# Kernel optimization log

Hardware: AMD Instinct MI355X
Metric: run time of the kernel (lower is better)

Reference implementation:

```python
import jax, jax.numpy as jnp
import numpy as np

B, S, D = 8, 2048, 512
KD = 64          # key_dim == value_dim
WIDTH = 128      # attention_width
NEG = 1.0e9


def setup_inputs() -> dict:
    key = jax.random.key(0)
    ks = jax.random.split(key, 16)
    glorot_dd = float(np.sqrt(6.0 / (D + KD)))
    glorot_sd = float(np.sqrt(6.0 / (S + KD)))
    u = lambda k, shape, lim: jax.random.uniform(k, shape, jnp.float32, -lim, lim)
    return {
        "x": jax.random.normal(ks[0], (B, S, D), jnp.float32),
        "Wqr": u(ks[1], (D, KD), glorot_dd), "bqr": jnp.zeros((KD,), jnp.float32),
        "Wqi": u(ks[2], (D, KD), glorot_dd), "bqi": jnp.zeros((KD,), jnp.float32),
        "Wkr": u(ks[3], (D, KD), glorot_dd), "bkr": jnp.zeros((KD,), jnp.float32),
        "Wki": u(ks[4], (D, KD), glorot_dd), "bki": jnp.zeros((KD,), jnp.float32),
        "Wv": u(ks[5], (D, KD), glorot_dd),  "bv": jnp.zeros((KD,), jnp.float32),
        "pos_qr": u(ks[6], (S, KD), glorot_sd), "pos_qi": u(ks[7], (S, KD), glorot_sd),
        "pos_kr": u(ks[8], (S, KD), glorot_sd), "pos_ki": u(ks[9], (S, KD), glorot_sd),
        "temperature": jnp.ones((1,), jnp.float32),
    }


def _masks():
    ind = jnp.arange(S)
    band = (jnp.abs(ind[:, None] - ind[None, :]) <= WIDTH).astype(jnp.float32)  # [S,S]
    causal = jnp.tril(jnp.ones((S, S), jnp.float32))                            # [S,S]
    return band, causal


def reference(x, Wqr, bqr, Wqi, bqi, Wkr, bkr, Wki, bki, Wv, bv,
              pos_qr, pos_qi, pos_kr, pos_ki, temperature):
    scale = 1.0 / jnp.sqrt(jnp.float32(KD))
    # complex Q/K via two real Dense layers; Q scaled BEFORE adding interference
    qr = (x @ Wqr + bqr) * scale + pos_qr[None]   # [B,S,KD]
    qi = (x @ Wqi + bqi) * scale + pos_qi[None]
    kr = (x @ Wkr + bkr) + pos_kr[None]
    ki = (x @ Wki + bki) + pos_ki[None]
    v = x @ Wv + bv                                # [B,S,KD]
    # real part of complex Q @ K^T (transpose, not conjugate-transpose)
    scores = (jnp.einsum('bsd,btd->bst', qr, kr)
              - jnp.einsum('bsd,btd->bst', qi, ki)) * scale  # [B,S,S]
    band, causal = _masks()
    scores = scores * band - NEG * (1.0 - band)
    scores = scores * causal - NEG * (1.0 - causal)
    probs = jax.nn.softmax(scores * temperature[0], axis=-1)
    return jnp.einsum('bst,btd->bsd', probs, v)
```

## Files before the change

kernel.cpp:

```cpp
#include <hip/hip_runtime.h>

#define NB 8
#define NS 2048
#define ND 512
#define NKD 64
#define NM (NB*NS)

typedef _Float16 f16x8 __attribute__((ext_vector_type(8)));
typedef float f32x4 __attribute__((ext_vector_type(4)));


__global__ __launch_bounds__(256) void wprep_kernel(
    const float* __restrict__ w0, const float* __restrict__ w1,
    const float* __restrict__ w2, const float* __restrict__ w3,
    const float* __restrict__ w4,
    f16x8* __restrict__ wfrag)
{
    const int t = blockIdx.x * 256 + threadIdx.x;
    const int p    = t >> 12;
    const int nf   = (t >> 10) & 3;
    const int kt   = (t >> 6) & 15;
    const int lane = t & 63;
    const float* __restrict__ W = (p==0)?w0:(p==1)?w1:(p==2)?w2:(p==3)?w3:w4;
    const int n  = nf*16 + (lane & 15);
    const int k0 = kt*32 + (lane >> 4)*8;
    f16x8 v;
    #pragma unroll
    for (int j = 0; j < 8; ++j)
        v[j] = (_Float16)W[(size_t)(k0 + j)*NKD + n];
    wfrag[t] = v;
}

__global__ __launch_bounds__(256) void proj_mfma(
    const float* __restrict__ x,
    const f16x8* __restrict__ wfrag,
    const float* __restrict__ b0, const float* __restrict__ b1,
    const float* __restrict__ b2, const float* __restrict__ b3,
    const float* __restrict__ b4,
    const float* __restrict__ p0, const float* __restrict__ p1,
    const float* __restrict__ p2, const float* __restrict__ p3,
    _Float16* __restrict__ qkri,
    _Float16* __restrict__ vT)
{
    const int g    = (blockIdx.x * 256 + threadIdx.x) >> 6;
    const int lane = threadIdx.x & 63;
    const int m0   = g * 16;

    const int row = m0 + (lane & 15);
    const int kb  = (lane >> 4) * 8;
    const float* __restrict__ xrow = x + (size_t)row * ND + kb;
    const f16x8* __restrict__ wf   = wfrag + lane;

    f32x4 acc[5][4];
    #pragma unroll
    for (int p = 0; p < 5; ++p)
        #pragma unroll
        for (int nf = 0; nf < 4; ++nf) acc[p][nf] = (f32x4){0.f,0.f,0.f,0.f};

    for (int kt = 0; kt < 16; ++kt) {
        float4 xa = *(const float4*)(xrow + kt*32);
        float4 xb = *(const float4*)(xrow + kt*32 + 4);
        f16x8 a;
        a[0]=(_Float16)xa.x; a[1]=(_Float16)xa.y;
        a[2]=(_Float16)xa.z; a[3]=(_Float16)xa.w;
        a[4]=(_Float16)xb.x; a[5]=(_Float16)xb.y;
        a[6]=(_Float16)xb.z; a[7]=(_Float16)xb.w;
        #pragma unroll
        for (int p = 0; p < 5; ++p)
            #pragma unroll
            for (int nf = 0; nf < 4; ++nf) {
                f16x8 b = wf[(p*4 + nf)*1024 + kt*64];
                acc[p][nf] = __builtin_amdgcn_mfma_f32_16x16x32_f16(a, b, acc[p][nf], 0, 0, 0);
            }
    }

    const float* biases[5] = {b0, b1, b2, b3, b4};
    const float* poss[4]   = {p0, p1, p2, p3};

    const int col   = lane & 15;
    const int rbase = (lane >> 4) << 2;
    const int bidx  = m0 >> 11;

    #pragma unroll
    for (int p = 0; p < 4; ++p) {
        _Float16* ob = qkri + ((size_t)p*NM + m0) * NKD;
        #pragma unroll
        for (int nf = 0; nf < 4; ++nf) {
            const int c = nf*16 + col;
            const float bb = biases[p][c];
            #pragma unroll
            for (int r = 0; r < 4; ++r) {
                const int mm = rbase + r;
                const int s  = (m0 + mm) & (NS - 1);
                float t = acc[p][nf][r] + bb;
                if (p < 2) t = t * 0.125f + poss[p][s*NKD + c];
                else       t = t + poss[p][s*NKD + c];
                ob[(size_t)mm*NKD + c] = (_Float16)t;
            }
        }
    }
    {
        _Float16* vb = vT + (size_t)bidx*NKD*NS;
        #pragma unroll
        for (int nf = 0; nf < 4; ++nf) {
            const int c = nf*16 + col;
            const float bb = b4[c];
            #pragma unroll
            for (int r = 0; r < 4; ++r) {
                const int s = (m0 + rbase + r) & (NS - 1);
                vb[(size_t)c*NS + s] = (_Float16)(acc[4][nf][r] + bb);
            }
        }
    }
}

#define PSTR 200

__global__ __launch_bounds__(64) void attn_mfma(
    const _Float16* __restrict__ qkri,
    const _Float16* __restrict__ vT,
    const float* __restrict__ temp,
    float* __restrict__ out)
{
    __shared__ _Float16 pl[16 * PSTR];

    const int lane = threadIdx.x;
    const int i0   = blockIdx.x * 16;
    const int b    = blockIdx.y;
    const int jb   = i0 - 128;

    const _Float16* __restrict__ qr_g = qkri + ((size_t)0*NM + (size_t)b*NS)*NKD;
    const _Float16* __restrict__ qi_g = qkri + ((size_t)1*NM + (size_t)b*NS)*NKD;
    const _Float16* __restrict__ kr_g = qkri + ((size_t)2*NM + (size_t)b*NS)*NKD;
    const _Float16* __restrict__ ki_g = qkri + ((size_t)3*NM + (size_t)b*NS)*NKD;
    const _Float16* __restrict__ vT_b = vT + (size_t)b*NKD*NS;

    const int qrow = i0 + (lane & 15);
    const int d0   = (lane >> 4) * 8;
    f16x8 aqr[2], aqi[2];
    #pragma unroll
    for (int kt = 0; kt < 2; ++kt) {
        aqr[kt] = *(const f16x8*)&qr_g[(size_t)qrow*NKD + kt*32 + d0];
        f16x8 qi8 = *(const f16x8*)&qi_g[(size_t)qrow*NKD + kt*32 + d0];
        aqi[kt] = -qi8;
    }

    const f16x8 zf = {};
    f32x4 st[9];
    #pragma unroll
    for (int t = 0; t < 9; ++t) {
        const int row = jb + 16*t + (lane & 15);
        const bool ok = (row >= 0);
        const _Float16* krp = kr_g + (size_t)row*NKD + d0;
        const _Float16* kip = ki_g + (size_t)row*NKD + d0;
        f16x8 bkr0 = ok ? *(const f16x8*)(krp)      : zf;
        f16x8 bkr1 = ok ? *(const f16x8*)(krp + 32) : zf;
        f16x8 bki0 = ok ? *(const f16x8*)(kip)      : zf;
        f16x8 bki1 = ok ? *(const f16x8*)(kip + 32) : zf;
        f32x4 acc = (f32x4){0.f,0.f,0.f,0.f};
        acc = __builtin_amdgcn_mfma_f32_16x16x32_f16(aqr[0], bkr0, acc, 0,0,0);
        acc = __builtin_amdgcn_mfma_f32_16x16x32_f16(aqr[1], bkr1, acc, 0,0,0);
        acc = __builtin_amdgcn_mfma_f32_16x16x32_f16(aqi[0], bki0, acc, 0,0,0);
        acc = __builtin_amdgcn_mfma_f32_16x16x32_f16(aqi[1], bki1, acc, 0,0,0);
        st[t] = acc;
    }

    const float sT  = 0.125f * temp[0];
    const int col   = lane & 15;
    const int qg4   = (lane >> 4) * 4;
    const int jrmin = -jb;
    float mx[4] = {-3e38f, -3e38f, -3e38f, -3e38f};
    #pragma unroll
    for (int t = 0; t < 9; ++t) {
        const int jr = 16*t + col;
        #pragma unroll
        for (int r = 0; r < 4; ++r) {
            const int row16 = qg4 + r;
            const bool ok = (jr >= row16) && (jr <= 128 + row16) && (jr >= jrmin);
            const float s = ok ? st[t][r]*sT : -1e30f;
            st[t][r] = s;
            mx[r] = fmaxf(mx[r], s);
        }
    }
    #pragma unroll
    for (int off = 1; off < 16; off <<= 1)
        #pragma unroll
        for (int r = 0; r < 4; ++r)
            mx[r] = fmaxf(mx[r], __shfl_xor(mx[r], off, 16));

    float sum[4] = {0.f, 0.f, 0.f, 0.f};
    #pragma unroll
    for (int t = 0; t < 9; ++t)
        #pragma unroll
        for (int r = 0; r < 4; ++r) {
            const float e = __expf(st[t][r] - mx[r]);
            st[t][r] = e;
            sum[r] += e;
        }
    #pragma unroll
    for (int off = 1; off < 16; off <<= 1)
        #pragma unroll
        for (int r = 0; r < 4; ++r)
            sum[r] += __shfl_xor(sum[r], off, 16);
    float inv[4];
    #pragma unroll
    for (int r = 0; r < 4; ++r) inv[r] = 1.0f / sum[r];

    #pragma unroll
    for (int t = 0; t < 9; ++t) {
        const int jr = 16*t + col;
        #pragma unroll
        for (int r = 0; r < 4; ++r)
            pl[(qg4 + r)*PSTR + jr] = (_Float16)(st[t][r] * inv[r]);
    }
    #pragma unroll
    for (int r = 0; r < 4; ++r)
        pl[(qg4 + r)*PSTR + 144 + col] = (_Float16)0.f;
    __syncthreads();

    f32x4 oacc[4];
    #pragma unroll
    for (int nf = 0; nf < 4; ++nf) oacc[nf] = (f32x4){0.f,0.f,0.f,0.f};
    const _Float16* pa = pl + (lane & 15)*PSTR + (lane >> 4)*8;
    #pragma unroll
    for (int kt = 0; kt < 5; ++kt) {
        f16x8 a = *(const f16x8*)(pa + kt*32);
        const int k0 = jb + kt*32 + (lane >> 4)*8;
        const bool okv = (k0 >= 0);
        #pragma unroll
        for (int nf = 0; nf < 4; ++nf) {
            const int d = nf*16 + (lane & 15);
            f16x8 bv = okv ? *(const f16x8*)&vT_b[(size_t)d*NS + k0] : zf;
            oacc[nf] = __builtin_amdgcn_mfma_f32_16x16x32_f16(a, bv, oacc[nf], 0,0,0);
        }
    }

    float* ob = out + ((size_t)b*NS + i0)*NKD;
    #pragma unroll
    for (int nf = 0; nf < 4; ++nf)
        #pragma unroll
        for (int r = 0; r < 4; ++r)
            ob[(size_t)(qg4 + r)*NKD + nf*16 + col] = oacc[nf][r];
}

extern "C" void kernel_launch(void* const* d_in, const int* in_sizes, int n_in,
                              void* d_out, int out_size, void* d_ws, size_t ws_size,
                              hipStream_t stream)
{
    const float* x    = (const float*)d_in[0];
    const float* w0   = (const float*)d_in[1];
    const float* b0   = (const float*)d_in[2];
    const float* w1   = (const float*)d_in[3];
    const float* b1   = (const float*)d_in[4];
    const float* w2   = (const float*)d_in[5];
    const float* b2   = (const float*)d_in[6];
    const float* w3   = (const float*)d_in[7];
    const float* b3   = (const float*)d_in[8];
    const float* w4   = (const float*)d_in[9];
    const float* b4   = (const float*)d_in[10];
    const float* p0   = (const float*)d_in[11];
    const float* p1   = (const float*)d_in[12];
    const float* p2   = (const float*)d_in[13];
    const float* p3   = (const float*)d_in[14];
    const float* temp = (const float*)d_in[15];

    char* ws = (char*)d_ws;
    f16x8*    wfrag = (f16x8*)ws;
    _Float16* qkri  = (_Float16*)(ws + 327680);
    _Float16* vT    = (_Float16*)(ws + 327680 + 8388608);

    wprep_kernel<<<80, 256, 0, stream>>>(w0, w1, w2, w3, w4, wfrag);

    proj_mfma<<<256, 256, 0, stream>>>(x, wfrag,
                                       b0, b1, b2, b3, b4,
                                       p0, p1, p2, p3, qkri, vT);

    dim3 gB(NS/16, NB);
    attn_mfma<<<gB, 64, 0, stream>>>(qkri, vT, temp, (float*)d_out);
}
```

Measured before the change: 46.71 us.

## Split attention block across four waves with LDS score exchange and reduction

Each attention block now runs four wavefronts instead of one. The 9 score tiles and the 5 PV k-steps are divided among the waves. Scores go to shared memory as fp32, every wave recomputes the row max and sum from LDS, and partial PV outputs are summed through LDS by wave 0. The aim is more parallelism and shorter per-wave serial MFMA chains, at the cost of extra LDS traffic, two barriers and redundant softmax-statistics work.

```diff
diff --git a/kernel.cpp b/kernel.cpp
--- a/kernel.cpp
+++ b/kernel.cpp
@@ -114,17 +114,21 @@
     }
 }
 
-#define PSTR 200
-
-__global__ __launch_bounds__(64) void attn_mfma(
+#define SST 164
+#define OST 68
+
+__global__ __launch_bounds__(256) void attn_mfma(
     const _Float16* __restrict__ qkri,
     const _Float16* __restrict__ vT,
     const float* __restrict__ temp,
     float* __restrict__ out)
 {
-    __shared__ _Float16 pl[16 * PSTR];
-
-    const int lane = threadIdx.x;
+    __shared__ __align__(16) float scf[16*SST];
+    __shared__ __align__(16) float olds[3][16*OST];
+
+    const int tid  = threadIdx.x;
+    const int w    = tid >> 6;
+    const int lane = tid & 63;
     const int i0   = blockIdx.x * 16;
     const int b    = blockIdx.y;
     const int jb   = i0 - 128;
@@ -135,8 +139,13 @@
     const _Float16* __restrict__ ki_g = qkri + ((size_t)3*NM + (size_t)b*NS)*NKD;
     const _Float16* __restrict__ vT_b = vT + (size_t)b*NKD*NS;
 
-    const int qrow = i0 + (lane & 15);
-    const int d0   = (lane >> 4) * 8;
+    const f16x8 zf = {};
+    const int col  = lane & 15;
+    const int seg  = lane >> 4;
+    const int qg4  = seg * 4;
+
+    const int qrow = i0 + col;
+    const int d0   = seg * 8;
     f16x8 aqr[2], aqi[2];
     #pragma unroll
     for (int kt = 0; kt < 2; ++kt) {
@@ -145,11 +154,13 @@
         aqi[kt] = -qi8;
     }
 
-    const f16x8 zf = {};
-    f32x4 st[9];
-    #pragma unroll
-    for (int t = 0; t < 9; ++t) {
-        const int row = jb + 16*t + (lane & 15);
+    const float sT  = 0.125f * temp[0];
+    const int jrmin = -jb;
+    const int tA = (w == 0) ? 0 : (2*w + 1);
+    const int tB = 2*w + 2;
+
+    for (int t = tA; t <= tB; ++t) {
+        const int row = jb + 16*t + col;
         const bool ok = (row >= 0);
         const _Float16* krp = kr_g + (size_t)row*NKD + d0;
         const _Float16* kip = ki_g + (size_t)row*NKD + d0;
@@ -162,85 +173,90 @@
         acc = __builtin_amdgcn_mfma_f32_16x16x32_f16(aqr[1], bkr1, acc, 0,0,0);
         acc = __builtin_amdgcn_mfma_f32_16x16x32_f16(aqi[0], bki0, acc, 0,0,0);
         acc = __builtin_amdgcn_mfma_f32_16x16x32_f16(aqi[1], bki1, acc, 0,0,0);
-        st[t] = acc;
-    }
-
-    const float sT  = 0.125f * temp[0];
-    const int col   = lane & 15;
-    const int qg4   = (lane >> 4) * 4;
-    const int jrmin = -jb;
-    float mx[4] = {-3e38f, -3e38f, -3e38f, -3e38f};
-    #pragma unroll
-    for (int t = 0; t < 9; ++t) {
         const int jr = 16*t + col;
         #pragma unroll
         for (int r = 0; r < 4; ++r) {
             const int row16 = qg4 + r;
-            const bool ok = (jr >= row16) && (jr <= 128 + row16) && (jr >= jrmin);
-            const float s = ok ? st[t][r]*sT : -1e30f;
-            st[t][r] = s;
-            mx[r] = fmaxf(mx[r], s);
-        }
-    }
-    #pragma unroll
-    for (int off = 1; off < 16; off <<= 1)
+            const bool okm = (jr >= row16) && (jr <= 128 + row16) && (jr >= jrmin);
+            scf[(qg4 + r)*SST + jr] = okm ? acc[r]*sT : -1e30f;
+        }
+    }
+    if (w == 0) {
         #pragma unroll
         for (int r = 0; r < 4; ++r)
-            mx[r] = fmaxf(mx[r], __shfl_xor(mx[r], off, 16));
-
-    float sum[4] = {0.f, 0.f, 0.f, 0.f};
-    #pragma unroll
-    for (int t = 0; t < 9; ++t)
-        #pragma unroll
-        for (int r = 0; r < 4; ++r) {
-            const float e = __expf(st[t][r] - mx[r]);
-            st[t][r] = e;
-            sum[r] += e;
-        }
-    #pragma unroll
-    for (int off = 1; off < 16; off <<= 1)
-        #pragma unroll
-        for (int r = 0; r < 4; ++r)
-            sum[r] += __shfl_xor(sum[r], off, 16);
-    float inv[4];
-    #pragma unroll
-    for (int r = 0; r < 4; ++r) inv[r] = 1.0f / sum[r];
-
-    #pragma unroll
-    for (int t = 0; t < 9; ++t) {
-        const int jr = 16*t + col;
-        #pragma unroll
-        for (int r = 0; r < 4; ++r)
-            pl[(qg4 + r)*PSTR + jr] = (_Float16)(st[t][r] * inv[r]);
-    }
-    #pragma unroll
-    for (int r = 0; r < 4; ++r)
-        pl[(qg4 + r)*PSTR + 144 + col] = (_Float16)0.f;
+            scf[(qg4 + r)*SST + 144 + col] = -1e30f;
+    }
     __syncthreads();
 
+    const float* srow = &scf[col*SST + seg*40];
+    float4 vv[10];
+    float m = -3e38f;
+    #pragma unroll
+    for (int c = 0; c < 10; ++c) {
+        vv[c] = *(const float4*)(srow + 4*c);
+        m = fmaxf(m, fmaxf(fmaxf(vv[c].x, vv[c].y), fmaxf(vv[c].z, vv[c].w)));
+    }
+    m = fmaxf(m, __shfl_xor(m, 16));
+    m = fmaxf(m, __shfl_xor(m, 32));
+    float l = 0.f;
+    #pragma unroll
+    for (int c = 0; c < 10; ++c) {
+        l += __expf(vv[c].x - m) + __expf(vv[c].y - m)
+           + __expf(vv[c].z - m) + __expf(vv[c].w - m);
+    }
+    l += __shfl_xor(l, 16);
+    l += __shfl_xor(l, 32);
+    const float inv = 1.0f / l;
+
     f32x4 oacc[4];
     #pragma unroll
     for (int nf = 0; nf < 4; ++nf) oacc[nf] = (f32x4){0.f,0.f,0.f,0.f};
-    const _Float16* pa = pl + (lane & 15)*PSTR + (lane >> 4)*8;
-    #pragma unroll
-    for (int kt = 0; kt < 5; ++kt) {
-        f16x8 a = *(const f16x8*)(pa + kt*32);
-        const int k0 = jb + kt*32 + (lane >> 4)*8;
-        const bool okv = (k0 >= 0);
+
+    #pragma unroll
+    for (int pass = 0; pass < 2; ++pass) {
+        const int kt = (pass == 0) ? w : 4;
+        if (pass == 1 && w != 0) break;
+        const int sb = 32*kt + seg*8;
+        float4 e0 = *(const float4*)&scf[col*SST + sb];
+        float4 e1 = *(const float4*)&scf[col*SST + sb + 4];
+        f16x8 a;
+        a[0] = (_Float16)(__expf(e0.x - m) * inv);
+        a[1] = (_Float16)(__expf(e0.y - m) * inv);
+        a[2] = (_Float16)(__expf(e0.z - m) * inv);
+        a[3] = (_Float16)(__expf(e0.w - m) * inv);
+        a[4] = (_Float16)(__expf(e1.x - m) * inv);
+        a[5] = (_Float16)(__expf(e1.y - m) * inv);
+        a[6] = (_Float16)(__expf(e1.z - m) * inv);
+        a[7] = (_Float16)(__expf(e1.w - m) * inv);
+        const int k0 = jb + 32*kt + seg*8;
+        const bool okv = (k0 >= 0) && (k0 <= NS - 8);
         #pragma unroll
         for (int nf = 0; nf < 4; ++nf) {
-            const int d = nf*16 + (lane & 15);
+            const int d = nf*16 + col;
             f16x8 bv = okv ? *(const f16x8*)&vT_b[(size_t)d*NS + k0] : zf;
             oacc[nf] = __builtin_amdgcn_mfma_f32_16x16x32_f16(a, bv, oacc[nf], 0,0,0);
         }
     }
 
-    float* ob = out + ((size_t)b*NS + i0)*NKD;
-    #pragma unroll
-    for (int nf = 0; nf < 4; ++nf)
-        #pragma unroll
-        for (int r = 0; r < 4; ++r)
-            ob[(size_t)(qg4 + r)*NKD + nf*16 + col] = oacc[nf][r];
+    if (w > 0) {
+        #pragma unroll
+        for (int nf = 0; nf < 4; ++nf)
+            #pragma unroll
+            for (int r = 0; r < 4; ++r)
+                olds[w-1][(qg4 + r)*OST + nf*16 + col] = oacc[nf][r];
+    }
+    __syncthreads();
+    if (w == 0) {
+        float* ob = out + ((size_t)b*NS + i0)*NKD;
+        #pragma unroll
+        for (int nf = 0; nf < 4; ++nf)
+            #pragma unroll
+            for (int r = 0; r < 4; ++r) {
+                const int idx = (qg4 + r)*OST + nf*16 + col;
+                const float v = oacc[nf][r] + olds[0][idx] + olds[1][idx] + olds[2][idx];
+                ob[(size_t)(qg4 + r)*NKD + nf*16 + col] = v;
+            }
+    }
 }
 
 extern "C" void kernel_launch(void* const* d_in, const int* in_sizes, int n_in,
@@ -276,5 +292,5 @@
                                        p0, p1, p2, p3, qkri, vT);
 
     dim3 gB(NS/16, NB);
-    attn_mfma<<<gB, 64, 0, stream>>>(qkri, vT, temp, (float*)d_out);
-}
+    attn_mfma<<<gB, 256, 0, stream>>>(qkri, vT, temp, (float*)d_out);
+}
```

New measurement: 43.77 us. 1.07x faster.
